# Optimization experiments

Measured on AMD Instinct MI355X. Metric: run time of the kernel, lower is better.

## Reference

```python
import jax, jax.numpy as jnp
import numpy as np

H_SIZE = 768
N_HEADS = 12
HEAD = H_SIZE // N_HEADS
INTER = 3072
N_LAYERS = 6
VOCAB = 65536
WIDTH = 512  # attention_width
EPS = 1e-6


def rmsnorm(x, w):
    return x * jax.lax.rsqrt(jnp.mean(x * x, axis=-1, keepdims=True) + EPS) * w


def rotate_every_two(x):
    # interleaved rotation: (x0,x1,x2,x3,...) -> (-x1,x0,-x3,x2,...)
    x1 = x[..., ::2]
    x2 = x[..., 1::2]
    return jnp.stack((-x2, x1), axis=-1).reshape(x.shape)


def fixed_pos_embedding(ages, dim):
    # ages: [B,S] float32 -> sin,cos: [B,S,1,dim]
    inv_freq = 1.0 / 10000 ** jnp.linspace(0.0, 2.0, dim // 2)
    t = ages[..., None] * inv_freq  # [B,S,dim//2]
    sin, cos = jnp.sin(t), jnp.cos(t)
    shp = ages.shape + (1, dim)
    sin = jnp.stack((sin, sin), axis=-1).reshape(shp)
    cos = jnp.stack((cos, cos), axis=-1).reshape(shp)
    return sin, cos


def local_attention(q, k, v, width):
    # causal local attention: query i attends to keys j with i-width < j <= i
    B, S, H, D = q.shape
    nb = S // width
    qb = q.reshape(B, nb, width, H, D)
    pad = ((0, 0), (width, 0), (0, 0), (0, 0))
    kp = jnp.pad(k, pad).reshape(B, nb + 1, width, H, D)
    vp = jnp.pad(v, pad).reshape(B, nb + 1, width, H, D)
    k2 = jnp.concatenate((kp[:, :-1], kp[:, 1:]), axis=2)  # [B,nb,2W,H,D]
    v2 = jnp.concatenate((vp[:, :-1], vp[:, 1:]), axis=2)
    scale = 1.0 / jnp.sqrt(jnp.asarray(D, q.dtype))
    scores = jnp.einsum('bnqhd,bnkhd->bnhqk', qb, k2) * scale
    qi = jnp.arange(width)[:, None]
    kj = jnp.arange(2 * width)[None, :]
    blk = jnp.arange(nb)[:, None, None]
    # global: i = b*W+qi, j = b*W - W + kj ; valid: j<=i, i-j<W, j>=0
    valid = (kj > qi) & (kj <= qi + width) & ((blk * width - width + kj) >= 0)
    scores = jnp.where(valid[None, :, None, :, :], scores, -jnp.inf)
    attn = jax.nn.softmax(scores, axis=-1)
    out = jnp.einsum('bnhqk,bnkhd->bnqhd', attn, v2)
    return out.reshape(B, S, H, D)


def encoder_layer(x, sin, cos, p):
    B, S, _ = x.shape
    xn = rmsnorm(x, p['norm_w'])
    qkv = (xn @ p['attn_W'] + p['attn_b']).reshape(B, S, 3, N_HEADS, HEAD)
    q = qkv[:, :, 0] * cos + rotate_every_two(qkv[:, :, 0]) * sin
    k = qkv[:, :, 1] * cos + rotate_every_two(qkv[:, :, 1]) * sin
    v = qkv[:, :, 2]
    attn = local_attention(q, k, v, WIDTH).reshape(B, S, H_SIZE)
    ff = jax.nn.gelu(xn @ p['in_W'] + p['in_b'], approximate=False)
    combined = jnp.concatenate((attn, ff), axis=-1)
    return combined @ p['out_W'] + p['out_b']


def setup_inputs() -> dict:
    key = jax.random.key(0)
    ks = jax.random.split(key, 10)
    B, S = 4, 2048
    std = 0.02
    tokens = jax.random.randint(ks[0], (B, S), 0, VOCAB, dtype=jnp.int64 if jax.config.jax_enable_x64 else jnp.int32)
    ages = jax.random.uniform(ks[1], (B, S), dtype=jnp.float32) * 1000.0
    embed = jax.random.normal(ks[2], (VOCAB, H_SIZE), jnp.float32) * std
    in_norm_w = jnp.ones((H_SIZE,), jnp.float32)
    out_norm_w = jnp.ones((H_SIZE,), jnp.float32)
    norm_w = jnp.ones((N_LAYERS, H_SIZE), jnp.float32)
    attn_W = jax.random.normal(ks[3], (N_LAYERS, H_SIZE, 3 * H_SIZE), jnp.float32) * std
    attn_b = jnp.zeros((N_LAYERS, 3 * H_SIZE), jnp.float32)
    in_W = jax.random.normal(ks[4], (N_LAYERS, H_SIZE, INTER), jnp.float32) * std
    in_b = jnp.zeros((N_LAYERS, INTER), jnp.float32)
    out_W = jax.random.normal(ks[5], (N_LAYERS, H_SIZE + INTER, H_SIZE), jnp.float32) * std
    out_b = jnp.zeros((N_LAYERS, H_SIZE), jnp.float32)
    return {'tokens': tokens, 'ages': ages, 'embed': embed,
            'in_norm_w': in_norm_w, 'out_norm_w': out_norm_w, 'norm_w': norm_w,
            'attn_W': attn_W, 'attn_b': attn_b, 'in_W': in_W, 'in_b': in_b,
            'out_W': out_W, 'out_b': out_b}


def reference(tokens, ages, embed, in_norm_w, out_norm_w, norm_w, attn_W, attn_b, in_W, in_b, out_W, out_b):
    x = embed[tokens]
    x = rmsnorm(x, in_norm_w)
    sin, cos = fixed_pos_embedding(ages, HEAD)
    params = {'norm_w': norm_w, 'attn_W': attn_W, 'attn_b': attn_b,
              'in_W': in_W, 'in_b': in_b, 'out_W': out_W, 'out_b': out_b}

    def step(h, p):
        return h + encoder_layer(h, sin, cos, p), None

    x, _ = jax.lax.scan(step, x, params)
    return rmsnorm(x, out_norm_w)
```

## Files before the change

kernel.cpp:

```cpp
#include <hip/hip_runtime.h>
#include <hip/hip_bf16.h>
#include <math.h>

#define H_SIZE 768
#define N_HEADS 12
#define HEAD 64
#define INTER 3072
#define N_LAYERS 6
#define BATCH 4
#define SEQ 2048
#define BS (BATCH*SEQ)
#define EPSV 1e-6f

typedef __attribute__((ext_vector_type(8))) short bf16x8;
typedef __attribute__((ext_vector_type(4))) float f32x4;
typedef unsigned short u16;

__device__ inline float bf2f(u16 v) {
    union { float f; unsigned u; } x; x.u = ((unsigned)v) << 16; return x.f;
}
__device__ inline u16 f2bf(float f) {
    union { float f; unsigned u; } x; x.f = f;
    unsigned u = x.u;
    return (u16)((u + 0x7FFFu + ((u >> 16) & 1u)) >> 16);
}

__device__ __forceinline__ void stage16(const u16* g, u16* ldsbase) {
    __builtin_amdgcn_global_load_lds((const __attribute__((address_space(1))) void*)g,
                                     (__attribute__((address_space(3))) void*)ldsbase,
                                     16, 0, 0);
}

__global__ void probe_kernel(const u16* __restrict__ embed, const int* __restrict__ tokens,
                             int* __restrict__ flags) {
    if (threadIdx.x == 0 && blockIdx.x == 0) {
        int good = 0, evenzero = 0;
        for (int i = 0; i < 128; i++) {
            u16 h = embed[i];
            int e = (h >> 7) & 0xFF;
            if (h == 0 || (e >= 87 && e <= 133)) good++;
            if ((i & 1) == 0 && h == 0) evenzero++;
        }
        flags[0] = (evenzero >= 48) ? 1 : ((good >= 110) ? 0 : 1);
        int z = 0;
        for (int i = 0; i < 64; i++) if (tokens[2 * i + 1] == 0) z++;
        flags[1] = (z >= 60) ? 1 : 0;
    }
}

__global__ __launch_bounds__(256) void sincos_kernel(const void* __restrict__ ages,
                                                     float* __restrict__ SIN,
                                                     float* __restrict__ COS,
                                                     const int* __restrict__ flags) {
    int idx = blockIdx.x * 256 + threadIdx.x;
    if (idx >= BS * 32) return;
    bool f32in = flags[0] != 0;
    int row = idx >> 5, f = idx & 31;
    float age = f32in ? ((const float*)ages)[row] : bf2f(((const u16*)ages)[row]);
    float inv = expf(-(2.0f * (float)f / 31.0f) * 9.210340371976184f);
    float t = age * inv;
    SIN[idx] = sinf(t);
    COS[idx] = cosf(t);
}

__global__ __launch_bounds__(256) void wtrans_kernel(const void* __restrict__ Wsrc,
                                                     u16* __restrict__ Wt,
                                                     int K, int N, size_t ltstride,
                                                     const int* __restrict__ flags) {
    __shared__ u16 tile[64][72];
    bool f32in = flags[0] != 0;
    int l = blockIdx.z;
    const float* W32 = (const float*)Wsrc + (size_t)l * K * N;
    const u16*   W16 = (const u16*)Wsrc + (size_t)l * K * N;
    u16* out = Wt + (size_t)l * ltstride;
    int k0 = blockIdx.y * 64, n0 = blockIdx.x * 64;
    int t = threadIdx.x;
    int kk = t >> 3, nn = (t & 7) * 8;
#pragma unroll
    for (int it = 0; it < 2; it++) {
        int kr = kk + it * 32;
        u16 tmp[8];
        if (f32in) {
            const float* src = W32 + (size_t)(k0 + kr) * N + n0 + nn;
            float4 f0 = *(const float4*)src, f1 = *(const float4*)(src + 4);
            tmp[0] = f2bf(f0.x); tmp[1] = f2bf(f0.y); tmp[2] = f2bf(f0.z); tmp[3] = f2bf(f0.w);
            tmp[4] = f2bf(f1.x); tmp[5] = f2bf(f1.y); tmp[6] = f2bf(f1.z); tmp[7] = f2bf(f1.w);
        } else {
            uint4 v = *(const uint4*)(W16 + (size_t)(k0 + kr) * N + n0 + nn);
            const u16* pv = (const u16*)&v;
#pragma unroll
            for (int i = 0; i < 8; i++) tmp[i] = pv[i];
        }
        *(uint4*)(&tile[kr][nn]) = *(const uint4*)tmp;
    }
    __syncthreads();
    int n = t >> 3, kq = (t & 7) * 8;
#pragma unroll
    for (int it = 0; it < 2; it++) {
        int nr = n + it * 32;
        u16 tmp[8];
#pragma unroll
        for (int i = 0; i < 8; i++) tmp[i] = tile[kq + i][nr];
        *(uint4*)(out + (size_t)(n0 + nr) * K + k0 + kq) = *(const uint4*)tmp;
    }
}

__global__ __launch_bounds__(256) void bias_conv_kernel(const void* __restrict__ ab,
                                                        const void* __restrict__ ib,
                                                        const void* __restrict__ ob,
                                                        u16* __restrict__ dst,
                                                        const int* __restrict__ flags) {
    int i = blockIdx.x * 256 + threadIdx.x;
    bool f32in = flags[0] != 0;
    const int A = 6 * 2304, B = 6 * 3072, C = 6 * 768;
    if (i < A) dst[i] = f32in ? f2bf(((const float*)ab)[i]) : ((const u16*)ab)[i];
    else if (i < A + B) { int j = i - A; dst[i] = f32in ? f2bf(((const float*)ib)[j]) : ((const u16*)ib)[j]; }
    else if (i < A + B + C) { int j = i - A - B; dst[i] = f32in ? f2bf(((const float*)ob)[j]) : ((const u16*)ob)[j]; }
}

__global__ __launch_bounds__(256) void embed_norm_kernel(const int* __restrict__ tokens,
                                                         const void* __restrict__ embed,
                                                         const void* __restrict__ wbase,
                                                         float* __restrict__ X,
                                                         const int* __restrict__ flags) {
    int row = blockIdx.x * 4 + (threadIdx.x >> 6);
    int lane = threadIdx.x & 63;
    bool f32in = flags[0] != 0;
    bool i64 = flags[1] != 0;
    int tok = i64 ? tokens[2 * row] : tokens[row];
    tok &= 65535;
    const u16* er16 = (const u16*)embed + (size_t)tok * H_SIZE;
    const float* er32 = (const float*)embed + (size_t)tok * H_SIZE;
    const u16* w16 = (const u16*)wbase;
    const float* w32 = (const float*)wbase;
    float v[12]; float ss = 0.f;
#pragma unroll
    for (int k = 0; k < 12; k++) {
        int i = lane + k * 64;
        float t = f32in ? er32[i] : bf2f(er16[i]);
        v[k] = t; ss += t * t;
    }
#pragma unroll
    for (int off = 1; off < 64; off <<= 1) ss += __shfl_xor(ss, off, 64);
    float scale = rsqrtf(ss * (1.0f / 768.0f) + EPSV);
#pragma unroll
    for (int k = 0; k < 12; k++) {
        int i = lane + k * 64;
        float wv = f32in ? w32[i] : bf2f(w16[i]);
        X[(size_t)row * H_SIZE + i] = v[k] * scale * wv;
    }
}

__global__ __launch_bounds__(256) void rmsnorm_kernel(const float* __restrict__ X,
                                                      const void* __restrict__ wbase, size_t woff,
                                                      void* __restrict__ Y, int outMode,
                                                      const int* __restrict__ flags) {
    int row = blockIdx.x * 4 + (threadIdx.x >> 6);
    int lane = threadIdx.x & 63;
    bool f32in = flags[0] != 0;
    const u16* w16 = (const u16*)wbase + woff;
    const float* w32 = (const float*)wbase + woff;
    const float* xr = X + (size_t)row * H_SIZE;
    float v[12]; float ss = 0.f;
#pragma unroll
    for (int k = 0; k < 12; k++) { v[k] = xr[lane + k * 64]; ss += v[k] * v[k]; }
#pragma unroll
    for (int off = 1; off < 64; off <<= 1) ss += __shfl_xor(ss, off, 64);
    float scale = rsqrtf(ss * (1.0f / 768.0f) + EPSV);
    bool of32 = outMode && f32in;
#pragma unroll
    for (int k = 0; k < 12; k++) {
        int i = lane + k * 64;
        float wv = f32in ? w32[i] : bf2f(w16[i]);
        float val = v[k] * scale * wv;
        if (of32) ((float*)Y)[(size_t)row * H_SIZE + i] = val;
        else      ((u16*)Y)[(size_t)row * H_SIZE + i] = f2bf(val);
    }
}

template <int EPI, int BN, int MGRP>
__global__ __launch_bounds__(256) void gemm_kernel(const u16* __restrict__ A,
                                                   const u16* __restrict__ Wt,
                                                   const u16* __restrict__ abias,
                                                   const u16* __restrict__ bbias,
                                                   float* __restrict__ Cf,
                                                   u16* __restrict__ qkvb,
                                                   u16* __restrict__ combb,
                                                   int K,
                                                   const float* __restrict__ SIN,
                                                   const float* __restrict__ COS) {
    constexpr int NF = BN / 32;
    __shared__ u16 Al[3][128][32];
    __shared__ u16 Bl[3][BN][32];
    const int tid = threadIdx.x;
    const int lane = tid & 63, wave = tid >> 6;
    const int wm = wave >> 1, wn = wave & 1;
    const int lm = lane & 15, g = lane >> 4;

    const int nx = gridDim.x;
    const int mpx = gridDim.y >> 3;
    int linear = blockIdx.y * nx + blockIdx.x;
    const int xcd = linear & 7;
    int wch = linear >> 3;
    const int grpsz = MGRP * nx;
    int grp = wch / grpsz;
    int rem = wch - grp * grpsz;
    int n_idx = rem / MGRP;
    int m_loc = grp * MGRP + (rem - n_idx * MGRP);
    const int m0 = (xcd * mpx + m_loc) * 128;
    const int n0 = n_idx * BN;

    f32x4 acc[4][NF];
#pragma unroll
    for (int i = 0; i < 4; i++)
#pragma unroll
        for (int j = 0; j < NF; j++) acc[i][j] = (f32x4)0.0f;

    const int swcol = ((lane & 3) ^ ((lane >> 3) & 3)) * 8;
    const u16* ga = A  + (size_t)(m0 + wave * 16 + (lane >> 2)) * K + swcol;
    const u16* gb = Wt + (size_t)(n0 + wave * 16 + (lane >> 2)) * K + swcol;
    const size_t row64 = (size_t)64 * K;

    auto STAGE = [&](int bi, int kk) {
        stage16(ga + kk, &Al[bi][wave * 16][0]);
        stage16(ga + row64 + kk, &Al[bi][64 + wave * 16][0]);
        stage16(gb + kk, &Bl[bi][wave * 16][0]);
        if constexpr (BN == 128) stage16(gb + row64 + kk, &Bl[bi][64 + wave * 16][0]);
    };

    STAGE(0, 0);
    STAGE(1, 32);
    int cur = 0;
    const int cc = (g ^ ((lm >> 1) & 3)) * 8;
    for (int k0 = 0; k0 < K; k0 += 32) {
        if (k0 + 32 < K) {
            if constexpr (BN == 128) asm volatile("s_waitcnt vmcnt(4)" ::: "memory");
            else                     asm volatile("s_waitcnt vmcnt(3)" ::: "memory");
        } else {
            asm volatile("s_waitcnt vmcnt(0)" ::: "memory");
        }
        __builtin_amdgcn_s_barrier();
        if (k0 + 64 < K) {
            int nx2 = cur + 2; if (nx2 >= 3) nx2 -= 3;
            STAGE(nx2, k0 + 64);
        }
        bf16x8 a[4], b[NF];
#pragma unroll
        for (int i = 0; i < 4; i++) a[i] = *(const bf16x8*)(&Al[cur][wm * 64 + i * 16 + lm][cc]);
#pragma unroll
        for (int j = 0; j < NF; j++) b[j] = *(const bf16x8*)(&Bl[cur][wn * (BN / 2) + j * 16 + lm][cc]);
#pragma unroll
        for (int i = 0; i < 4; i++)
#pragma unroll
            for (int j = 0; j < NF; j++)
                acc[i][j] = __builtin_amdgcn_mfma_f32_16x16x32_bf16(a[i], b[j], acc[i][j], 0, 0, 0);
        cur += 1; if (cur >= 3) cur = 0;
    }

#pragma unroll
    for (int i = 0; i < 4; i++) {
        int mbase = m0 + wm * 64 + i * 16 + g * 4;
#pragma unroll
        for (int j = 0; j < NF; j++) {
            int n = n0 + wn * (BN / 2) + j * 16 + lm;
            float bv;
            if (EPI == 0) bv = (n < 2304) ? bf2f(abias[n]) : bf2f(bbias[n - 2304]);
            else          bv = bf2f(abias[n]);
#pragma unroll
            for (int r = 0; r < 4; r++) {
                float v = acc[i][j][r] + bv;
                int mm = mbase + r;
                if (EPI == 0) {
                    float p = __shfl_xor(v, 1);
                    if (n < 2304) {
                        float outv = v;
                        if (n < 1536) {
                            int f = (n >> 1) & 31;
                            float c = COS[mm * 32 + f], s = SIN[mm * 32 + f];
                            outv = (n & 1) ? (v * c + p * s) : (v * c - p * s);
                        }
                        qkvb[(size_t)mm * 2304 + n] = f2bf(outv);
                    } else {
                        float u = 0.7978845608f * (v + 0.044715f * v * v * v);
                        float e = __expf(2.0f * u);
                        float th = 1.0f - 2.0f / (e + 1.0f);
                        combb[(size_t)mm * 3840 + (n - 1536)] = f2bf(0.5f * v * (1.0f + th));
                    }
                } else {
                    Cf[(size_t)mm * 768 + n] += v;
                }
            }
        }
    }
}

__global__ __launch_bounds__(256) void attn_kernel(const u16* __restrict__ qkv,
                                                   u16* __restrict__ Out) {
    __shared__ u16 Qs[64][72];
    __shared__ u16 Ks[64][72];
    __shared__ u16 Vt[64][72];
    __shared__ u16 Ps[4][16][72];

    const int tid = threadIdx.x;
    const int lane = tid & 63, wave = tid >> 6;
    const int lm = lane & 15, g = lane >> 4;
    const int q0 = blockIdx.x * 64;
    const int h = blockIdx.y;
    const int b = blockIdx.z;
    const size_t rowbase = (size_t)b * SEQ;

#pragma unroll
    for (int it = 0; it < 2; ++it) {
        int idx = tid + it * 256;
        int r = idx >> 3, u = (idx & 7) * 8;
        uint4 v = *(const uint4*)(qkv + (rowbase + q0 + r) * 2304 + h * HEAD + u);
        *(uint4*)(&Qs[r][u]) = v;
    }

    float m_r[4], l_r[4];
    f32x4 o[4];
#pragma unroll
    for (int r = 0; r < 4; r++) { m_r[r] = -INFINITY; l_r[r] = 0.f; }
#pragma unroll
    for (int d = 0; d < 4; d++) o[d] = (f32x4)0.0f;

    const int c_start = (q0 < 512) ? ((512 - q0) >> 6) : 0;
    for (int c = c_start; c < 9; ++c) {
        int kc = q0 - 512 + c * 64;
        __syncthreads();
#pragma unroll
        for (int it = 0; it < 2; ++it) {
            int idx = tid + it * 256;
            int r = idx >> 3, u = (idx & 7) * 8;
            int j = kc + r;
            uint4 kv = make_uint4(0, 0, 0, 0), vv = make_uint4(0, 0, 0, 0);
            if (j >= 0) {
                kv = *(const uint4*)(qkv + (rowbase + j) * 2304 + 768 + h * HEAD + u);
                vv = *(const uint4*)(qkv + (rowbase + j) * 2304 + 1536 + h * HEAD + u);
            }
            *(uint4*)(&Ks[r][u]) = kv;
            const u16* pv = (const u16*)&vv;
#pragma unroll
            for (int i = 0; i < 8; i++) Vt[u + i][r] = pv[i];
        }
        __syncthreads();

        bf16x8 aq0 = *(const bf16x8*)(&Qs[wave * 16 + lm][g * 8]);
        bf16x8 aq1 = *(const bf16x8*)(&Qs[wave * 16 + lm][32 + g * 8]);
        f32x4 s[4];
#pragma unroll
        for (int kf = 0; kf < 4; kf++) {
            bf16x8 b0 = *(const bf16x8*)(&Ks[kf * 16 + lm][g * 8]);
            bf16x8 b1 = *(const bf16x8*)(&Ks[kf * 16 + lm][32 + g * 8]);
            f32x4 z = (f32x4)0.0f;
            z = __builtin_amdgcn_mfma_f32_16x16x32_bf16(aq0, b0, z, 0, 0, 0);
            z = __builtin_amdgcn_mfma_f32_16x16x32_bf16(aq1, b1, z, 0, 0, 0);
            s[kf] = z;
        }

        float sv[4][4], mc[4];
#pragma unroll
        for (int r = 0; r < 4; r++) mc[r] = -INFINITY;
#pragma unroll
        for (int kf = 0; kf < 4; kf++) {
            int j = kc + kf * 16 + lm;
#pragma unroll
            for (int r = 0; r < 4; r++) {
                int i = q0 + wave * 16 + g * 4 + r;
                bool valid = (j >= 0) && (j <= i) && (j >= i - 511);
                float v = valid ? s[kf][r] * 0.125f : -INFINITY;
                sv[kf][r] = v;
                mc[r] = fmaxf(mc[r], v);
            }
        }
#pragma unroll
        for (int off = 1; off < 16; off <<= 1)
#pragma unroll
            for (int r = 0; r < 4; r++) mc[r] = fmaxf(mc[r], __shfl_xor(mc[r], off, 64));

        float alpha[4], mn[4];
#pragma unroll
        for (int r = 0; r < 4; r++) {
            mn[r] = fmaxf(m_r[r], mc[r]);
            alpha[r] = (mn[r] > -1e37f) ? __expf(m_r[r] - mn[r]) : 1.0f;
            m_r[r] = mn[r];
        }
        float ps[4][4], rs[4] = {0.f, 0.f, 0.f, 0.f};
#pragma unroll
        for (int kf = 0; kf < 4; kf++)
#pragma unroll
            for (int r = 0; r < 4; r++) {
                float p = (sv[kf][r] > -1e37f) ? __expf(sv[kf][r] - mn[r]) : 0.0f;
                ps[kf][r] = p;
                rs[r] += p;
            }
#pragma unroll
        for (int off = 1; off < 16; off <<= 1)
#pragma unroll
            for (int r = 0; r < 4; r++) rs[r] += __shfl_xor(rs[r], off, 64);
#pragma unroll
        for (int r = 0; r < 4; r++) l_r[r] = l_r[r] * alpha[r] + rs[r];

#pragma unroll
        for (int kf = 0; kf < 4; kf++)
#pragma unroll
            for (int r = 0; r < 4; r++) Ps[wave][g * 4 + r][kf * 16 + lm] = f2bf(ps[kf][r]);

#pragma unroll
        for (int d = 0; d < 4; d++)
#pragma unroll
            for (int r = 0; r < 4; r++) o[d][r] *= alpha[r];

        bf16x8 pa0 = *(const bf16x8*)(&Ps[wave][lm][g * 8]);
        bf16x8 pa1 = *(const bf16x8*)(&Ps[wave][lm][32 + g * 8]);
#pragma unroll
        for (int d = 0; d < 4; d++) {
            bf16x8 b0 = *(const bf16x8*)(&Vt[d * 16 + lm][g * 8]);
            bf16x8 b1 = *(const bf16x8*)(&Vt[d * 16 + lm][32 + g * 8]);
            o[d] = __builtin_amdgcn_mfma_f32_16x16x32_bf16(pa0, b0, o[d], 0, 0, 0);
            o[d] = __builtin_amdgcn_mfma_f32_16x16x32_bf16(pa1, b1, o[d], 0, 0, 0);
        }
    }

#pragma unroll
    for (int d = 0; d < 4; d++) {
        int dd = d * 16 + lm;
#pragma unroll
        for (int r = 0; r < 4; r++) {
            int i = q0 + wave * 16 + g * 4 + r;
            float v = o[d][r] / l_r[r];
            Out[(rowbase + i) * 3840 + h * HEAD + dd] = f2bf(v);
        }
    }
}

extern "C" void kernel_launch(void* const* d_in, const int* in_sizes, int n_in,
                              void* d_out, int out_size, void* d_ws, size_t ws_size,
                              hipStream_t stream) {
    const int* tokens   = (const int*)d_in[0];
    const void* ages    = d_in[1];
    const void* embed   = d_in[2];
    const void* in_norm_w  = d_in[3];
    const void* out_norm_w = d_in[4];
    const void* norm_w     = d_in[5];
    const void* attn_W     = d_in[6];
    const void* attn_b     = d_in[7];
    const void* in_W       = d_in[8];
    const void* in_b       = d_in[9];
    const void* out_W      = d_in[10];
    const void* out_b      = d_in[11];

    char* w = (char*)d_ws;
    int* flags  = (int*)w;   w += 256;
    float* x    = (float*)w; w += (size_t)BS * H_SIZE * 4;
    u16* xn     = (u16*)w;   w += (size_t)BS * H_SIZE * 2;
    u16* qkv    = (u16*)w;   w += (size_t)BS * 2304 * 2;
    u16* comb   = (u16*)w;   w += (size_t)BS * 3840 * 2;
    float* sinb = (float*)w; w += (size_t)BS * 32 * 4;
    float* cosb = (float*)w; w += (size_t)BS * 32 * 4;
    u16* wtf    = (u16*)w;   w += (size_t)N_LAYERS * 5376 * 768 * 2;
    u16* wto    = (u16*)w;   w += (size_t)N_LAYERS * 768 * 3840 * 2;
    u16* biasb  = (u16*)w;   w += (size_t)(6*2304 + 6*3072 + 6*768) * 2;

    u16* ab_b = biasb;
    u16* ib_b = biasb + 6 * 2304;
    u16* ob_b = ib_b + 6 * 3072;

    const size_t LFS = (size_t)5376 * 768;

    probe_kernel<<<1, 64, 0, stream>>>((const u16*)embed, tokens, flags);
    sincos_kernel<<<(BS * 32 + 255) / 256, 256, 0, stream>>>(ages, sinb, cosb, flags);
    embed_norm_kernel<<<BS / 4, 256, 0, stream>>>(tokens, embed, in_norm_w, x, flags);
    bias_conv_kernel<<<(6 * (2304 + 3072 + 768) + 255) / 256, 256, 0, stream>>>(
        attn_b, in_b, out_b, biasb, flags);

    wtrans_kernel<<<dim3(2304 / 64, 768 / 64, N_LAYERS), 256, 0, stream>>>(
        attn_W, wtf, 768, 2304, LFS, flags);
    wtrans_kernel<<<dim3(3072 / 64, 768 / 64, N_LAYERS), 256, 0, stream>>>(
        in_W, wtf + (size_t)2304 * 768, 768, 3072, LFS, flags);
    wtrans_kernel<<<dim3(768 / 64, 3840 / 64, N_LAYERS), 256, 0, stream>>>(
        out_W, wto, 3840, 768, (size_t)768 * 3840, flags);

    for (int l = 0; l < N_LAYERS; ++l) {
        rmsnorm_kernel<<<BS / 4, 256, 0, stream>>>(x, norm_w, (size_t)l * H_SIZE, xn, 0, flags);
        gemm_kernel<0, 128, 8><<<dim3(5376 / 128, BS / 128), 256, 0, stream>>>(
            xn, wtf + (size_t)l * LFS, ab_b + l * 2304, ib_b + l * 3072,
            nullptr, qkv, comb, H_SIZE, sinb, cosb);
        attn_kernel<<<dim3(SEQ / 64, N_HEADS, BATCH), 256, 0, stream>>>(qkv, comb);
        gemm_kernel<2, 64, 4><<<dim3(768 / 64, BS / 128), 256, 0, stream>>>(
            comb, wto + (size_t)l * 768 * 3840, ob_b + l * 768, nullptr,
            x, nullptr, nullptr, H_SIZE + INTER, nullptr, nullptr);
    }
    rmsnorm_kernel<<<BS / 4, 256, 0, stream>>>(x, out_norm_w, 0, d_out, 1, flags);
}
```

Measured before the change: 1.791 ms.

## Use 256x256 eight-wave tiles for QKV/FFN-in GEMM and raise MFMA priority

Generalizes the GEMM kernel over BM and wave count so the fused QKV/FFN-in GEMM runs 256x256 tiles with 512 threads (8 waves). Each tile now reuses more A and B data per LDS load. Staging and vmcnt waits are re-derived from the tile parameters, and s_setprio brackets the MFMA block to favour math issue over loads. The cost is a larger LDS footprint (one block per CU) and higher register pressure. There are also far fewer blocks (672), which can cause tail imbalance across CUs.

```diff
diff --git a/kernel.cpp b/kernel.cpp
--- a/kernel.cpp
+++ b/kernel.cpp
@@ -178,19 +178,26 @@
     }
 }
 
-template <int EPI, int BN, int MGRP>
-__global__ __launch_bounds__(256) void gemm_kernel(const u16* __restrict__ A,
-                                                   const u16* __restrict__ Wt,
-                                                   const u16* __restrict__ abias,
-                                                   const u16* __restrict__ bbias,
-                                                   float* __restrict__ Cf,
-                                                   u16* __restrict__ qkvb,
-                                                   u16* __restrict__ combb,
-                                                   int K,
-                                                   const float* __restrict__ SIN,
-                                                   const float* __restrict__ COS) {
-    constexpr int NF = BN / 32;
-    __shared__ u16 Al[3][128][32];
+template <int EPI, int BM, int BN, int MGRP>
+__global__ __launch_bounds__(BM == 256 ? 512 : 256)
+void gemm_kernel(const u16* __restrict__ A,
+                 const u16* __restrict__ Wt,
+                 const u16* __restrict__ abias,
+                 const u16* __restrict__ bbias,
+                 float* __restrict__ Cf,
+                 u16* __restrict__ qkvb,
+                 u16* __restrict__ combb,
+                 int K,
+                 const float* __restrict__ SIN,
+                 const float* __restrict__ COS) {
+    constexpr int WAVES = (BM == 256) ? 8 : 4;
+    constexpr int NJ = BN / 64;
+    constexpr int WaveN = BN / 2;
+    constexpr int NF = WaveN / 16;
+    constexpr int RB = BN / WAVES;
+    constexpr int LPS = 2 + RB / 16;
+    (void)NJ;
+    __shared__ u16 Al[3][BM][32];
     __shared__ u16 Bl[3][BN][32];
     const int tid = threadIdx.x;
     const int lane = tid & 63, wave = tid >> 6;
@@ -207,7 +214,7 @@
     int rem = wch - grp * grpsz;
     int n_idx = rem / MGRP;
     int m_loc = grp * MGRP + (rem - n_idx * MGRP);
-    const int m0 = (xcd * mpx + m_loc) * 128;
+    const int m0 = (xcd * mpx + m_loc) * BM;
     const int n0 = n_idx * BN;
 
     f32x4 acc[4][NF];
@@ -217,15 +224,14 @@
         for (int j = 0; j < NF; j++) acc[i][j] = (f32x4)0.0f;
 
     const int swcol = ((lane & 3) ^ ((lane >> 3) & 3)) * 8;
-    const u16* ga = A  + (size_t)(m0 + wave * 16 + (lane >> 2)) * K + swcol;
-    const u16* gb = Wt + (size_t)(n0 + wave * 16 + (lane >> 2)) * K + swcol;
-    const size_t row64 = (size_t)64 * K;
+    const u16* ga = A  + (size_t)(m0 + wave * (BM / WAVES) + (lane >> 2)) * K + swcol;
+    const u16* gb = Wt + (size_t)(n0 + wave * RB + (lane >> 2)) * K + swcol;
 
     auto STAGE = [&](int bi, int kk) {
-        stage16(ga + kk, &Al[bi][wave * 16][0]);
-        stage16(ga + row64 + kk, &Al[bi][64 + wave * 16][0]);
-        stage16(gb + kk, &Bl[bi][wave * 16][0]);
-        if constexpr (BN == 128) stage16(gb + row64 + kk, &Bl[bi][64 + wave * 16][0]);
+        stage16(ga + kk, &Al[bi][wave * (BM / WAVES)][0]);
+        stage16(ga + (size_t)16 * K + kk, &Al[bi][wave * (BM / WAVES) + 16][0]);
+        stage16(gb + kk, &Bl[bi][wave * RB][0]);
+        if constexpr (RB == 32) stage16(gb + (size_t)16 * K + kk, &Bl[bi][wave * RB + 16][0]);
     };
 
     STAGE(0, 0);
@@ -234,8 +240,7 @@
     const int cc = (g ^ ((lm >> 1) & 3)) * 8;
     for (int k0 = 0; k0 < K; k0 += 32) {
         if (k0 + 32 < K) {
-            if constexpr (BN == 128) asm volatile("s_waitcnt vmcnt(4)" ::: "memory");
-            else                     asm volatile("s_waitcnt vmcnt(3)" ::: "memory");
+            asm volatile("s_waitcnt vmcnt(%0)" :: "i"(LPS) : "memory");
         } else {
             asm volatile("s_waitcnt vmcnt(0)" ::: "memory");
         }
@@ -248,12 +253,14 @@
 #pragma unroll
         for (int i = 0; i < 4; i++) a[i] = *(const bf16x8*)(&Al[cur][wm * 64 + i * 16 + lm][cc]);
 #pragma unroll
-        for (int j = 0; j < NF; j++) b[j] = *(const bf16x8*)(&Bl[cur][wn * (BN / 2) + j * 16 + lm][cc]);
+        for (int j = 0; j < NF; j++) b[j] = *(const bf16x8*)(&Bl[cur][wn * WaveN + j * 16 + lm][cc]);
+        __builtin_amdgcn_s_setprio(1);
 #pragma unroll
         for (int i = 0; i < 4; i++)
 #pragma unroll
             for (int j = 0; j < NF; j++)
                 acc[i][j] = __builtin_amdgcn_mfma_f32_16x16x32_bf16(a[i], b[j], acc[i][j], 0, 0, 0);
+        __builtin_amdgcn_s_setprio(0);
         cur += 1; if (cur >= 3) cur = 0;
     }
 
@@ -262,7 +269,7 @@
         int mbase = m0 + wm * 64 + i * 16 + g * 4;
 #pragma unroll
         for (int j = 0; j < NF; j++) {
-            int n = n0 + wn * (BN / 2) + j * 16 + lm;
+            int n = n0 + wn * WaveN + j * 16 + lm;
             float bv;
             if (EPI == 0) bv = (n < 2304) ? bf2f(abias[n]) : bf2f(bbias[n - 2304]);
             else          bv = bf2f(abias[n]);
@@ -483,11 +490,11 @@
 
     for (int l = 0; l < N_LAYERS; ++l) {
         rmsnorm_kernel<<<BS / 4, 256, 0, stream>>>(x, norm_w, (size_t)l * H_SIZE, xn, 0, flags);
-        gemm_kernel<0, 128, 8><<<dim3(5376 / 128, BS / 128), 256, 0, stream>>>(
+        gemm_kernel<0, 256, 256, 4><<<dim3(5376 / 256, BS / 256), 512, 0, stream>>>(
             xn, wtf + (size_t)l * LFS, ab_b + l * 2304, ib_b + l * 3072,
             nullptr, qkv, comb, H_SIZE, sinb, cosb);
         attn_kernel<<<dim3(SEQ / 64, N_HEADS, BATCH), 256, 0, stream>>>(qkv, comb);
-        gemm_kernel<2, 64, 4><<<dim3(768 / 64, BS / 128), 256, 0, stream>>>(
+        gemm_kernel<2, 128, 64, 4><<<dim3(768 / 64, BS / 128), 256, 0, stream>>>(
             comb, wto + (size_t)l * 768 * 3840, ob_b + l * 768, nullptr,
             x, nullptr, nullptr, H_SIZE + INTER, nullptr, nullptr);
     }
```

Result: slower. 1.967 ms (+9.8%).
